# Kernel tuning notes

Measured on AMD Instinct MI355X. Metric: run time of the kernel, lower is better.

Reference implementation:

```python
import jax, jax.numpy as jnp
import numpy as np

EPS = 1e-8

def setup_inputs() -> dict:
    key = jax.random.key(0)
    kq, kk, kv = jax.random.split(key, 3)
    S, B, D = 2048, 8, 64
    return {
        "query": jax.random.normal(kq, (S, B, D), dtype=jnp.float32),
        "key": jax.random.normal(kk, (S, B, D), dtype=jnp.float32),
        "value": jax.random.normal(kv, (S, B, D), dtype=jnp.float32),
    }

def reference(query, key, value):
    # SWAP-test fidelity: expval(Z) = |<q_hat|k_hat>|^2, overlap = 0.5*(1+Z).
    # Zero-padding to 2**n_qubits does not change the inner product.
    q_hat = query / (jnp.linalg.norm(query, axis=-1, keepdims=True) + EPS)
    k_hat = key / (jnp.linalg.norm(key, axis=-1, keepdims=True) + EPS)
    # cosine similarity per batch: [B, S_q, S_k]
    cos = jnp.einsum('ibd,jbd->bij', q_hat, k_hat)
    overlap = 0.5 * (1.0 + cos * cos)
    attn_probs = jax.nn.softmax(overlap, axis=-1)          # [B, S, S]
    context = jnp.einsum('bij,jbd->ibd', attn_probs, value)  # [S, B, D]
    attn_weights = jnp.transpose(attn_probs, (1, 0, 2))      # [S, B, S]
    return context, attn_weights
```

## Files before the change

kernel.cpp:

```cpp
#include <hip/hip_runtime.h>

#define S_LEN 2048
#define BATCH 8
#define DIM   64
#define QT    16
#define KT    64
#define NT    32
#define NQT   128
#define PP    68
#define PBP   72
#define EPSV  1e-8f

#define WS_K_OFF (1u << 20)
#define WS_V_OFF (1u << 21)
#define WS_NEED_BYTES (6u * 1024u * 1024u)

typedef __attribute__((ext_vector_type(8))) short short8;
typedef __attribute__((ext_vector_type(4))) short short4v;
typedef __attribute__((ext_vector_type(4))) float f32x4;

__device__ __forceinline__ short bf16b(float x) {
    unsigned int u = __builtin_bit_cast(unsigned int, x);
    u = (u + 0x7fffu + ((u >> 16) & 1u)) >> 16;
    return (short)u;
}

__global__ __launch_bounds__(256)
void prep(const float* __restrict__ Qg, const float* __restrict__ Kg,
          const float* __restrict__ Vg, short* __restrict__ ws)
{
    const int blk = blockIdx.x;
    const int tid = threadIdx.x;
    if (blk < 512) {
        const bool isK = blk >= 256;
        const float* src = isK ? Kg : Qg;
        short* dst = ws + (isK ? WS_K_OFF : 0u);
        const int rg = (blk & 255) * 64 + (tid >> 2);
        const int rq = tid & 3;
        const int s = rg >> 3, b = rg & 7;
        const float4* rp = reinterpret_cast<const float4*>(src) + (size_t)rg * 16;
        float4 v[4];
        float ss = 0.f;
        #pragma unroll
        for (int c = 0; c < 4; ++c) {
            v[c] = rp[rq * 4 + c];
            ss += v[c].x*v[c].x + v[c].y*v[c].y + v[c].z*v[c].z + v[c].w*v[c].w;
        }
        ss += __shfl_xor(ss, 1);
        ss += __shfl_xor(ss, 2);
        const float sc = 1.f / (sqrtf(ss) + EPSV);
        const float* pf = reinterpret_cast<const float*>(v);
        #pragma unroll
        for (int h = 0; h < 2; ++h) {
            const int c8 = rq * 2 + h;
            const int kk = c8 >> 2, lg = c8 & 3;
            const int chunk = (b * NQT + (s >> 4)) * 128 + kk * 64 + lg * 16 + (s & 15);
            short8 o;
            #pragma unroll
            for (int j = 0; j < 8; ++j) o[j] = bf16b(pf[h * 8 + j] * sc);
            *reinterpret_cast<short8*>(dst + (size_t)chunk * 8) = o;
        }
    } else {
        const int cid = (blk - 512) * 256 + tid;
        const int l  = cid & 63;
        const int kk = (cid >> 6) & 1;
        const int gd = (cid >> 7) & 3;
        const int t  = (cid >> 9) & 31;
        const int b  = cid >> 14;
        const int d  = gd * 16 + (l & 15);
        const int k0 = t * 64 + kk * 32 + (l >> 4) * 8;
        short8 o;
        #pragma unroll
        for (int j = 0; j < 8; ++j)
            o[j] = bf16b(Vg[((size_t)(k0 + j) * BATCH + b) * DIM + d]);
        *reinterpret_cast<short8*>(ws + WS_V_OFF + (size_t)cid * 8) = o;
    }
}

__global__ __launch_bounds__(256, 4)
void qattn2(const short* __restrict__ Qp, const short* __restrict__ Kp,
            const short* __restrict__ Vp, float* __restrict__ out)
{
    __shared__ float Pf[QT * PP];
    __shared__ short Pb[QT * PBP];
    __shared__ float rsum[QT];

    const int tid = threadIdx.x;
    const int l   = tid & 63;
    const int w   = tid >> 6;
    const int lg  = l >> 4;
    const int lr  = l & 15;

    const int b     = blockIdx.x & 7;
    const int qt    = blockIdx.x >> 3;
    const int qbase = qt * QT;

    const short8* Qc = reinterpret_cast<const short8*>(Qp) + (size_t)(b * NQT + qt) * 128;
    const short8 aq0 = Qc[l];
    const short8 aq1 = Qc[64 + l];

    if (tid < QT) rsum[tid] = 0.f;
    __syncthreads();

    const short8* Kb = reinterpret_cast<const short8*>(Kp) + (size_t)b * NQT * 128;
    const short8* Vb = reinterpret_cast<const short8*>(Vp) + (size_t)b * NT * 4 * 128;

    float sums[4] = {0.f, 0.f, 0.f, 0.f};
    for (int t = 0; t < NT; ++t) {
        const short8* kc = Kb + (size_t)(4 * t + w) * 128 + l;
        const short8 k0 = kc[0];
        const short8 k1 = kc[64];
        f32x4 acc = {0.f, 0.f, 0.f, 0.f};
        acc = __builtin_amdgcn_mfma_f32_16x16x32_bf16(aq0, k0, acc, 0, 0, 0);
        acc = __builtin_amdgcn_mfma_f32_16x16x32_bf16(aq1, k1, acc, 0, 0, 0);
        #pragma unroll
        for (int r = 0; r < 4; ++r) {
            float c = acc[r];
            sums[r] += __expf(0.5f + 0.5f * c * c);
        }
    }
    #pragma unroll
    for (int r = 0; r < 4; ++r) {
        float v = sums[r];
        v += __shfl_xor(v, 1);
        v += __shfl_xor(v, 2);
        v += __shfl_xor(v, 4);
        v += __shfl_xor(v, 8);
        sums[r] = v;
    }
    if (lr == 0) {
        #pragma unroll
        for (int r = 0; r < 4; ++r)
            atomicAdd(&rsum[lg * 4 + r], sums[r]);
    }
    __syncthreads();
    float inv_[4];
    #pragma unroll
    for (int r = 0; r < 4; ++r) inv_[r] = 1.f / rsum[lg * 4 + r];

    float* attn = out + (size_t)S_LEN * BATCH * DIM;
    f32x4 cacc = {0.f, 0.f, 0.f, 0.f};

    short8 k0, k1;
    {
        const short8* kc = Kb + (size_t)w * 128 + l;
        k0 = kc[0]; k1 = kc[64];
    }

    for (int t = 0; t < NT; ++t) {
        const short8* vc = Vb + (size_t)(t * 4 + w) * 128 + l;
        const short8 v0 = vc[0];
        const short8 v1 = vc[64];
        const int tn = (t + 1 < NT) ? t + 1 : t;
        const short8* kc = Kb + (size_t)(4 * tn + w) * 128 + l;
        const short8 kn0 = kc[0];
        const short8 kn1 = kc[64];

        f32x4 acc = {0.f, 0.f, 0.f, 0.f};
        acc = __builtin_amdgcn_mfma_f32_16x16x32_bf16(aq0, k0, acc, 0, 0, 0);
        acc = __builtin_amdgcn_mfma_f32_16x16x32_bf16(aq1, k1, acc, 0, 0, 0);
        #pragma unroll
        for (int r = 0; r < 4; ++r) {
            float c = acc[r];
            float p = __expf(0.5f + 0.5f * c * c) * inv_[r];
            Pf[(lg * 4 + r) * PP + w * 16 + lr] = p;
            Pb[(lg * 4 + r) * PBP + w * 16 + lr] = bf16b(p);
        }
        asm volatile("s_waitcnt lgkmcnt(0)" ::: "memory");
        __builtin_amdgcn_sched_barrier(0);
        __builtin_amdgcn_s_barrier();
        __builtin_amdgcn_sched_barrier(0);

        const short8 ap0 = *reinterpret_cast<const short8*>(&Pb[lr * PBP + lg * 8]);
        const short8 ap1 = *reinterpret_cast<const short8*>(&Pb[lr * PBP + 32 + lg * 8]);
        cacc = __builtin_amdgcn_mfma_f32_16x16x32_bf16(ap0, v0, cacc, 0, 0, 0);
        cacc = __builtin_amdgcn_mfma_f32_16x16x32_bf16(ap1, v1, cacc, 0, 0, 0);

        {
            const int q  = tid >> 4;
            const int c4 = (tid & 15) * 4;
            f32x4 pv = *reinterpret_cast<const f32x4*>(&Pf[q * PP + c4]);
            __builtin_nontemporal_store(pv, reinterpret_cast<f32x4*>(
                attn + (size_t)(qbase + q) * (BATCH * S_LEN) + b * S_LEN + t * KT + c4));
        }
        asm volatile("s_waitcnt lgkmcnt(0)" ::: "memory");
        __builtin_amdgcn_sched_barrier(0);
        __builtin_amdgcn_s_barrier();
        __builtin_amdgcn_sched_barrier(0);

        k0 = kn0; k1 = kn1;
    }

    #pragma unroll
    for (int r = 0; r < 4; ++r) {
        out[(size_t)(qbase + lg * 4 + r) * (BATCH * DIM) + b * DIM + w * 16 + lr] = cacc[r];
    }
}

#define FQT 32
#define FQP 72
#define FPP 68

__global__ __launch_bounds__(256, 4)
void qattn_fb(const float* __restrict__ Qg, const float* __restrict__ Kg,
              const float* __restrict__ Vg, float* __restrict__ out)
{
    __shared__ short Qsh[FQT * FQP];
    __shared__ short Ksh[KT * FQP];
    __shared__ short VTs[DIM * FQP];
    __shared__ short Pb [FQT * FQP];
    __shared__ float Pf [FQT * FPP];
    __shared__ float rsum[FQT];

    const int tid = threadIdx.x;
    const int l   = tid & 63;
    const int w   = tid >> 6;
    const int lg  = l >> 4;
    const int lr  = l & 15;
    const int ms  = (w & 1) * 16;
    const int np  = (w >> 1) * 2;

    const int b     = blockIdx.x & 7;
    const int qtile = blockIdx.x >> 3;
    const int qbase = qtile * FQT;

    const int rr = tid >> 2;
    const int rq = tid & 3;

    if (tid < FQT * 4) {
        const float4* qp = reinterpret_cast<const float4*>(
            Qg + (size_t)(qbase + rr) * (BATCH * DIM) + b * DIM);
        float4 v[4];
        float ss = 0.f;
        #pragma unroll
        for (int c = 0; c < 4; ++c) {
            v[c] = qp[rq + 4 * c];
            ss += v[c].x*v[c].x + v[c].y*v[c].y + v[c].z*v[c].z + v[c].w*v[c].w;
        }
        ss += __shfl_xor(ss, 1);
        ss += __shfl_xor(ss, 2);
        const float sc = 1.f / (sqrtf(ss) + EPSV);
        #pragma unroll
        for (int c = 0; c < 4; ++c) {
            short4v s4 = { bf16b(v[c].x * sc), bf16b(v[c].y * sc),
                           bf16b(v[c].z * sc), bf16b(v[c].w * sc) };
            *reinterpret_cast<short4v*>(&Qsh[rr * FQP + rq * 4 + 16 * c]) = s4;
        }
    }
    if (tid < FQT) rsum[tid] = 0.f;
    __syncthreads();

    short8 aq[2];
    #pragma unroll
    for (int kk = 0; kk < 2; ++kk)
        aq[kk] = *reinterpret_cast<const short8*>(&Qsh[(ms + lr) * FQP + kk * 32 + lg * 8]);

    float sums[4] = {0.f, 0.f, 0.f, 0.f};
    for (int t = 0; t < NT; ++t) {
        __syncthreads();
        {
            const float4* kp = reinterpret_cast<const float4*>(
                Kg + (size_t)(t * KT + rr) * (BATCH * DIM) + b * DIM);
            float4 v[4];
            float ss = 0.f;
            #pragma unroll
            for (int c = 0; c < 4; ++c) {
                v[c] = kp[rq + 4 * c];
                ss += v[c].x*v[c].x + v[c].y*v[c].y + v[c].z*v[c].z + v[c].w*v[c].w;
            }
            ss += __shfl_xor(ss, 1);
            ss += __shfl_xor(ss, 2);
            const float sc = 1.f / (sqrtf(ss) + EPSV);
            #pragma unroll
            for (int c = 0; c < 4; ++c) {
                short4v s4 = { bf16b(v[c].x * sc), bf16b(v[c].y * sc),
                               bf16b(v[c].z * sc), bf16b(v[c].w * sc) };
                *reinterpret_cast<short4v*>(&Ksh[rr * FQP + rq * 4 + 16 * c]) = s4;
            }
        }
        __syncthreads();
        #pragma unroll
        for (int g = 0; g < 2; ++g) {
            f32x4 acc = {0.f, 0.f, 0.f, 0.f};
            #pragma unroll
            for (int kk = 0; kk < 2; ++kk) {
                short8 bk = *reinterpret_cast<const short8*>(
                    &Ksh[((np + g) * 16 + lr) * FQP + kk * 32 + lg * 8]);
                acc = __builtin_amdgcn_mfma_f32_16x16x32_bf16(aq[kk], bk, acc, 0, 0, 0);
            }
            #pragma unroll
            for (int r = 0; r < 4; ++r) {
                float c = acc[r];
                sums[r] += __expf(0.5f + 0.5f * c * c);
            }
        }
    }
    #pragma unroll
    for (int r = 0; r < 4; ++r) {
        float v = sums[r];
        v += __shfl_xor(v, 1);
        v += __shfl_xor(v, 2);
        v += __shfl_xor(v, 4);
        v += __shfl_xor(v, 8);
        sums[r] = v;
    }
    if (lr == 0) {
        #pragma unroll
        for (int r = 0; r < 4; ++r)
            atomicAdd(&rsum[ms + lg * 4 + r], sums[r]);
    }
    __syncthreads();
    float inv4[4];
    #pragma unroll
    for (int r = 0; r < 4; ++r)
        inv4[r] = 1.f / rsum[ms + lg * 4 + r];

    float* attn = out + (size_t)S_LEN * BATCH * DIM;
    f32x4 cacc[2];
    cacc[0] = (f32x4){0.f, 0.f, 0.f, 0.f};
    cacc[1] = (f32x4){0.f, 0.f, 0.f, 0.f};

    for (int t = 0; t < NT; ++t) {
        __syncthreads();
        {
            const float4* kp = reinterpret_cast<const float4*>(
                Kg + (size_t)(t * KT + rr) * (BATCH * DIM) + b * DIM);
            float4 v[4];
            float ss = 0.f;
            #pragma unroll
            for (int c = 0; c < 4; ++c) {
                v[c] = kp[rq + 4 * c];
                ss += v[c].x*v[c].x + v[c].y*v[c].y + v[c].z*v[c].z + v[c].w*v[c].w;
            }
            ss += __shfl_xor(ss, 1);
            ss += __shfl_xor(ss, 2);
            const float sc = 1.f / (sqrtf(ss) + EPSV);
            #pragma unroll
            for (int c = 0; c < 4; ++c) {
                short4v s4 = { bf16b(v[c].x * sc), bf16b(v[c].y * sc),
                               bf16b(v[c].z * sc), bf16b(v[c].w * sc) };
                *reinterpret_cast<short4v*>(&Ksh[rr * FQP + rq * 4 + 16 * c]) = s4;
            }
        }
        {
            const float4* vp = reinterpret_cast<const float4*>(
                Vg + (size_t)(t * KT + rr) * (BATCH * DIM) + b * DIM);
            #pragma unroll
            for (int c = 0; c < 4; ++c) {
                float4 v = vp[rq + 4 * c];
                int d0 = rq * 4 + 16 * c;
                VTs[(d0 + 0) * FQP + rr] = bf16b(v.x);
                VTs[(d0 + 1) * FQP + rr] = bf16b(v.y);
                VTs[(d0 + 2) * FQP + rr] = bf16b(v.z);
                VTs[(d0 + 3) * FQP + rr] = bf16b(v.w);
            }
        }
        __syncthreads();
        #pragma unroll
        for (int g = 0; g < 2; ++g) {
            f32x4 acc = {0.f, 0.f, 0.f, 0.f};
            #pragma unroll
            for (int kk = 0; kk < 2; ++kk) {
                short8 bk = *reinterpret_cast<const short8*>(
                    &Ksh[((np + g) * 16 + lr) * FQP + kk * 32 + lg * 8]);
                acc = __builtin_amdgcn_mfma_f32_16x16x32_bf16(aq[kk], bk, acc, 0, 0, 0);
            }
            #pragma unroll
            for (int r = 0; r < 4; ++r) {
                float c = acc[r];
                float p = __expf(0.5f + 0.5f * c * c) * inv4[r];
                int q_r = ms + lg * 4 + r;
                int k_c = (np + g) * 16 + lr;
                Pf[q_r * FPP + k_c] = p;
                Pb[q_r * FQP + k_c] = bf16b(p);
            }
        }
        __syncthreads();
        #pragma unroll
        for (int g = 0; g < 2; ++g) {
            #pragma unroll
            for (int kk = 0; kk < 2; ++kk) {
                short8 ap = *reinterpret_cast<const short8*>(
                    &Pb[(ms + lr) * FQP + kk * 32 + lg * 8]);
                short8 bv = *reinterpret_cast<const short8*>(
                    &VTs[((np + g) * 16 + lr) * FQP + kk * 32 + lg * 8]);
                cacc[g] = __builtin_amdgcn_mfma_f32_16x16x32_bf16(ap, bv, cacc[g], 0, 0, 0);
            }
        }
        #pragma unroll
        for (int s = 0; s < 2; ++s) {
            int q  = s * 16 + (tid >> 4);
            int c4 = (tid & 15) * 4;
            f32x4 pv = *reinterpret_cast<const f32x4*>(&Pf[q * FPP + c4]);
            __builtin_nontemporal_store(pv, reinterpret_cast<f32x4*>(
                attn + (size_t)(qbase + q) * (BATCH * S_LEN) + b * S_LEN + t * KT + c4));
        }
    }

    #pragma unroll
    for (int g = 0; g < 2; ++g) {
        #pragma unroll
        for (int r = 0; r < 4; ++r) {
            __builtin_nontemporal_store(cacc[g][r],
                out + (size_t)(qbase + ms + lg * 4 + r) * (BATCH * DIM)
                    + b * DIM + (np + g) * 16 + lr);
        }
    }
}

extern "C" void kernel_launch(void* const* d_in, const int* in_sizes, int n_in,
                              void* d_out, int out_size, void* d_ws, size_t ws_size,
                              hipStream_t stream)
{
    const float* q = (const float*)d_in[0];
    const float* k = (const float*)d_in[1];
    const float* v = (const float*)d_in[2];
    float* o  = (float*)d_out;

    if (ws_size >= WS_NEED_BYTES && d_ws != nullptr) {
        short* ws = (short*)d_ws;
        prep<<<1024, 256, 0, stream>>>(q, k, v, ws);
        qattn2<<<1024, 256, 0, stream>>>(ws, ws + WS_K_OFF, ws + WS_V_OFF, o);
    } else {
        qattn_fb<<<BATCH * (S_LEN / FQT), 256, 0, stream>>>(q, k, v, o);
    }
}
```

Baseline: 171.3 us.

## Enlarge attention tile to 32 queries x 128 keys with 8-wave blocks

Result: no change. 169.6 us (-1.0%).

```diff
diff --git a/kernel.cpp b/kernel.cpp
--- a/kernel.cpp
+++ b/kernel.cpp
@@ -3,12 +3,12 @@
 #define S_LEN 2048
 #define BATCH 8
 #define DIM   64
-#define QT    16
-#define KT    64
-#define NT    32
+#define QT    32
+#define KTILE 128
+#define NT2   16
 #define NQT   128
-#define PP    68
-#define PBP   72
+#define PP    132
+#define PBP   136
 #define EPSV  1e-8f
 
 #define WS_K_OFF (1u << 20)
@@ -24,6 +24,13 @@
     u = (u + 0x7fffu + ((u >> 16) & 1u)) >> 16;
     return (short)u;
 }
+
+#define LDS_BARRIER() do { \
+    asm volatile("s_waitcnt lgkmcnt(0)" ::: "memory"); \
+    __builtin_amdgcn_sched_barrier(0); \
+    __builtin_amdgcn_s_barrier(); \
+    __builtin_amdgcn_sched_barrier(0); \
+} while (0)
 
 __global__ __launch_bounds__(256)
 void prep(const float* __restrict__ Qg, const float* __restrict__ Kg,
@@ -77,8 +84,8 @@
     }
 }
 
-__global__ __launch_bounds__(256, 4)
-void qattn2(const short* __restrict__ Qp, const short* __restrict__ Kp,
+__global__ __launch_bounds__(512, 4)
+void qattn3(const short* __restrict__ Qp, const short* __restrict__ Kp,
             const short* __restrict__ Vp, float* __restrict__ out)
 {
     __shared__ float Pf[QT * PP];
@@ -90,33 +97,237 @@
     const int w   = tid >> 6;
     const int lg  = l >> 4;
     const int lr  = l & 15;
+    const int kg  = w;
+    const int ms  = (w >> 2) * 16;
+    const int dg  = w & 3;
 
     const int b     = blockIdx.x & 7;
     const int qt    = blockIdx.x >> 3;
     const int qbase = qt * QT;
 
-    const short8* Qc = reinterpret_cast<const short8*>(Qp) + (size_t)(b * NQT + qt) * 128;
-    const short8 aq0 = Qc[l];
-    const short8 aq1 = Qc[64 + l];
+    const short8* Qp8 = reinterpret_cast<const short8*>(Qp);
+    short8 aq[2][2];
+    #pragma unroll
+    for (int m = 0; m < 2; ++m) {
+        const size_t base = (size_t)(b * NQT + qt * 2 + m) * 128;
+        aq[m][0] = Qp8[base + l];
+        aq[m][1] = Qp8[base + 64 + l];
+    }
 
     if (tid < QT) rsum[tid] = 0.f;
     __syncthreads();
 
-    const short8* Kb = reinterpret_cast<const short8*>(Kp) + (size_t)b * NQT * 128;
-    const short8* Vb = reinterpret_cast<const short8*>(Vp) + (size_t)b * NT * 4 * 128;
+    const short8* Kb8 = reinterpret_cast<const short8*>(Kp) + (size_t)b * NQT * 128;
+    const short8* Vb8 = reinterpret_cast<const short8*>(Vp) + (size_t)b * 32 * 4 * 128;
+
+    float sums[2][4] = {{0.f,0.f,0.f,0.f},{0.f,0.f,0.f,0.f}};
+    short8 k0 = Kb8[(size_t)kg * 128 + l];
+    short8 k1 = Kb8[(size_t)kg * 128 + 64 + l];
+    for (int t = 0; t < NT2; ++t) {
+        const int tn = (t + 1 < NT2) ? t + 1 : t;
+        const short8* kc = &Kb8[(size_t)(8 * tn + kg) * 128 + l];
+        const short8 kn0 = kc[0];
+        const short8 kn1 = kc[64];
+        #pragma unroll
+        for (int m = 0; m < 2; ++m) {
+            f32x4 acc = {0.f, 0.f, 0.f, 0.f};
+            acc = __builtin_amdgcn_mfma_f32_16x16x32_bf16(aq[m][0], k0, acc, 0, 0, 0);
+            acc = __builtin_amdgcn_mfma_f32_16x16x32_bf16(aq[m][1], k1, acc, 0, 0, 0);
+            #pragma unroll
+            for (int r = 0; r < 4; ++r) {
+                float c = acc[r];
+                sums[m][r] += __expf(0.5f + 0.5f * c * c);
+            }
+        }
+        k0 = kn0; k1 = kn1;
+    }
+    #pragma unroll
+    for (int m = 0; m < 2; ++m)
+    #pragma unroll
+    for (int r = 0; r < 4; ++r) {
+        float v = sums[m][r];
+        v += __shfl_xor(v, 1);
+        v += __shfl_xor(v, 2);
+        v += __shfl_xor(v, 4);
+        v += __shfl_xor(v, 8);
+        sums[m][r] = v;
+    }
+    if (lr == 0) {
+        #pragma unroll
+        for (int m = 0; m < 2; ++m)
+        #pragma unroll
+        for (int r = 0; r < 4; ++r)
+            atomicAdd(&rsum[m * 16 + lg * 4 + r], sums[m][r]);
+    }
+    __syncthreads();
+    float inv_[2][4];
+    #pragma unroll
+    for (int m = 0; m < 2; ++m)
+    #pragma unroll
+    for (int r = 0; r < 4; ++r)
+        inv_[m][r] = 1.f / rsum[m * 16 + lg * 4 + r];
+
+    float* attn = out + (size_t)S_LEN * BATCH * DIM;
+    f32x4 cacc = {0.f, 0.f, 0.f, 0.f};
+
+    k0 = Kb8[(size_t)kg * 128 + l];
+    k1 = Kb8[(size_t)kg * 128 + 64 + l];
+
+    for (int t = 0; t < NT2; ++t) {
+        short8 bv[4];
+        #pragma unroll
+        for (int kk2 = 0; kk2 < 4; ++kk2) {
+            const int tv = t * 2 + (kk2 >> 1);
+            bv[kk2] = Vb8[(size_t)(tv * 4 + dg) * 128 + (kk2 & 1) * 64 + l];
+        }
+        const int tn = (t + 1 < NT2) ? t + 1 : t;
+        const short8* kc = &Kb8[(size_t)(8 * tn + kg) * 128 + l];
+        const short8 kn0 = kc[0];
+        const short8 kn1 = kc[64];
+
+        #pragma unroll
+        for (int m = 0; m < 2; ++m) {
+            f32x4 acc = {0.f, 0.f, 0.f, 0.f};
+            acc = __builtin_amdgcn_mfma_f32_16x16x32_bf16(aq[m][0], k0, acc, 0, 0, 0);
+            acc = __builtin_amdgcn_mfma_f32_16x16x32_bf16(aq[m][1], k1, acc, 0, 0, 0);
+            #pragma unroll
+            for (int r = 0; r < 4; ++r) {
+                float c = acc[r];
+                float p = __expf(0.5f + 0.5f * c * c) * inv_[m][r];
+                const int q_r = m * 16 + lg * 4 + r;
+                const int k_c = kg * 16 + lr;
+                Pf[q_r * PP + k_c] = p;
+                Pb[q_r * PBP + k_c] = bf16b(p);
+            }
+        }
+        LDS_BARRIER();
+
+        {
+            const int q = tid >> 4;
+            const int c = (tid & 15) * 4;
+            f32x4 pv0 = *reinterpret_cast<const f32x4*>(&Pf[q * PP + c]);
+            f32x4 pv1 = *reinterpret_cast<const f32x4*>(&Pf[q * PP + 64 + c]);
+            float* dst = attn + (size_t)(qbase + q) * (BATCH * S_LEN) + b * S_LEN + t * KTILE;
+            __builtin_nontemporal_store(pv0, reinterpret_cast<f32x4*>(dst + c));
+            __builtin_nontemporal_store(pv1, reinterpret_cast<f32x4*>(dst + 64 + c));
+        }
+
+        #pragma unroll
+        for (int kk2 = 0; kk2 < 4; ++kk2) {
+            const short8 ap = *reinterpret_cast<const short8*>(
+                &Pb[(ms + lr) * PBP + kk2 * 32 + lg * 8]);
+            cacc = __builtin_amdgcn_mfma_f32_16x16x32_bf16(ap, bv[kk2], cacc, 0, 0, 0);
+        }
+        LDS_BARRIER();
+
+        k0 = kn0; k1 = kn1;
+    }
+
+    #pragma unroll
+    for (int r = 0; r < 4; ++r) {
+        out[(size_t)(qbase + ms + lg * 4 + r) * (BATCH * DIM) + b * DIM + dg * 16 + lr]
+            = cacc[r];
+    }
+}
+
+#define FQT 32
+#define FQP 72
+#define FPP 68
+#define FKT 64
+#define FNT 32
+
+__global__ __launch_bounds__(256, 4)
+void qattn_fb(const float* __restrict__ Qg, const float* __restrict__ Kg,
+              const float* __restrict__ Vg, float* __restrict__ out)
+{
+    __shared__ short Qsh[FQT * FQP];
+    __shared__ short Ksh[FKT * FQP];
+    __shared__ short VTs[DIM * FQP];
+    __shared__ short Pb [FQT * FQP];
+    __shared__ float Pf [FQT * FPP];
+    __shared__ float rsum[FQT];
+
+    const int tid = threadIdx.x;
+    const int l   = tid & 63;
+    const int w   = tid >> 6;
+    const int lg  = l >> 4;
+    const int lr  = l & 15;
+    const int ms  = (w & 1) * 16;
+    const int np  = (w >> 1) * 2;
+
+    const int b     = blockIdx.x & 7;
+    const int qtile = blockIdx.x >> 3;
+    const int qbase = qtile * FQT;
+
+    const int rr = tid >> 2;
+    const int rq = tid & 3;
+
+    if (tid < FQT * 4) {
+        const float4* qp = reinterpret_cast<const float4*>(
+            Qg + (size_t)(qbase + rr) * (BATCH * DIM) + b * DIM);
+        float4 v[4];
+        float ss = 0.f;
+        #pragma unroll
+        for (int c = 0; c < 4; ++c) {
+            v[c] = qp[rq + 4 * c];
+            ss += v[c].x*v[c].x + v[c].y*v[c].y + v[c].z*v[c].z + v[c].w*v[c].w;
+        }
+        ss += __shfl_xor(ss, 1);
+        ss += __shfl_xor(ss, 2);
+        const float sc = 1.f / (sqrtf(ss) + EPSV);
+        #pragma unroll
+        for (int c = 0; c < 4; ++c) {
+            short4v s4 = { bf16b(v[c].x * sc), bf16b(v[c].y * sc),
+                           bf16b(v[c].z * sc), bf16b(v[c].w * sc) };
+            *reinterpret_cast<short4v*>(&Qsh[rr * FQP + rq * 4 + 16 * c]) = s4;
+        }
+    }
+    if (tid < FQT) rsum[tid] = 0.f;
+    __syncthreads();
+
+    short8 aq[2];
+    #pragma unroll
+    for (int kk = 0; kk < 2; ++kk)
+        aq[kk] = *reinterpret_cast<const short8*>(&Qsh[(ms + lr) * FQP + kk * 32 + lg * 8]);
 
     float sums[4] = {0.f, 0.f, 0.f, 0.f};
-    for (int t = 0; t < NT; ++t) {
-        const short8* kc = Kb + (size_t)(4 * t + w) * 128 + l;
-        const short8 k0 = kc[0];
-        const short8 k1 = kc[64];
-        f32x4 acc = {0.f, 0.f, 0.f, 0.f};
-        acc = __builtin_amdgcn_mfma_f32_16x16x32_bf16(aq0, k0, acc, 0, 0, 0);
-        acc = __builtin_amdgcn_mfma_f32_16x16x32_bf16(aq1, k1, acc, 0, 0, 0);
-        #pragma unroll
-        for (int r = 0; r < 4; ++r) {
-            float c = acc[r];
-            sums[r] += __expf(0.5f + 0.5f * c * c);
+    for (int t = 0; t < FNT; ++t) {
+        __syncthreads();
+        {
+            const float4* kp = reinterpret_cast<const float4*>(
+                Kg + (size_t)(t * FKT + rr) * (BATCH * DIM) + b * DIM);
+            float4 v[4];
+            float ss = 0.f;
+            #pragma unroll
+            for (int c = 0; c < 4; ++c) {
+                v[c] = kp[rq + 4 * c];
+                ss += v[c].x*v[c].x + v[c].y*v[c].y + v[c].z*v[c].z + v[c].w*v[c].w;
+            }
+            ss += __shfl_xor(ss, 1);
+            ss += __shfl_xor(ss, 2);
+            const float sc = 1.f / (sqrtf(ss) + EPSV);
+            #pragma unroll
+            for (int c = 0; c < 4; ++c) {
+                short4v s4 = { bf16b(v[c].x * sc), bf16b(v[c].y * sc),
+                               bf16b(v[c].z * sc), bf16b(v[c].w * sc) };
+                *reinterpret_cast<short4v*>(&Ksh[rr * FQP + rq * 4 + 16 * c]) = s4;
+            }
+        }
+        __syncthreads();
+        #pragma unroll
+        for (int g = 0; g < 2; ++g) {
+            f32x4 acc = {0.f, 0.f, 0.f, 0.f};
+            #pragma unroll
+            for (int kk = 0; kk < 2; ++kk) {
+                short8 bk = *reinterpret_cast<const short8*>(
+                    &Ksh[((np + g) * 16 + lr) * FQP + kk * 32 + lg * 8]);
+                acc = __builtin_amdgcn_mfma_f32_16x16x32_bf16(aq[kk], bk, acc, 0, 0, 0);
+            }
+            #pragma unroll
+            for (int r = 0; r < 4; ++r) {
+                float c = acc[r];
+                sums[r] += __expf(0.5f + 0.5f * c * c);
+            }
         }
     }
     #pragma unroll
@@ -131,136 +342,24 @@
     if (lr == 0) {
         #pragma unroll
         for (int r = 0; r < 4; ++r)
-            atomicAdd(&rsum[lg * 4 + r], sums[r]);
+            atomicAdd(&rsum[ms + lg * 4 + r], sums[r]);
     }
     __syncthreads();
-    float inv_[4];
-    #pragma unroll
-    for (int r = 0; r < 4; ++r) inv_[r] = 1.f / rsum[lg * 4 + r];
+    float inv4[4];
+    #pragma unroll
+    for (int r = 0; r < 4; ++r)
+        inv4[r] = 1.f / rsum[ms + lg * 4 + r];
 
     float* attn = out + (size_t)S_LEN * BATCH * DIM;
-    f32x4 cacc = {0.f, 0.f, 0.f, 0.f};
-
-    short8 k0, k1;
-    {
-        const short8* kc = Kb + (size_t)w * 128 + l;
-        k0 = kc[0]; k1 = kc[64];
-    }
-
-    for (int t = 0; t < NT; ++t) {
-        const short8* vc = Vb + (size_t)(t * 4 + w) * 128 + l;
-        const short8 v0 = vc[0];
-        const short8 v1 = vc[64];
-        const int tn = (t + 1 < NT) ? t + 1 : t;
-        const short8* kc = Kb + (size_t)(4 * tn + w) * 128 + l;
-        const short8 kn0 = kc[0];
-        const short8 kn1 = kc[64];
-
-        f32x4 acc = {0.f, 0.f, 0.f, 0.f};
-        acc = __builtin_amdgcn_mfma_f32_16x16x32_bf16(aq0, k0, acc, 0, 0, 0);
-        acc = __builtin_amdgcn_mfma_f32_16x16x32_bf16(aq1, k1, acc, 0, 0, 0);
-        #pragma unroll
-        for (int r = 0; r < 4; ++r) {
-            float c = acc[r];
-            float p = __expf(0.5f + 0.5f * c * c) * inv_[r];
-            Pf[(lg * 4 + r) * PP + w * 16 + lr] = p;
-            Pb[(lg * 4 + r) * PBP + w * 16 + lr] = bf16b(p);
-        }
-        asm volatile("s_waitcnt lgkmcnt(0)" ::: "memory");
-        __builtin_amdgcn_sched_barrier(0);
-        __builtin_amdgcn_s_barrier();
-        __builtin_amdgcn_sched_barrier(0);
-
-        const short8 ap0 = *reinterpret_cast<const short8*>(&Pb[lr * PBP + lg * 8]);
-        const short8 ap1 = *reinterpret_cast<const short8*>(&Pb[lr * PBP + 32 + lg * 8]);
-        cacc = __builtin_amdgcn_mfma_f32_16x16x32_bf16(ap0, v0, cacc, 0, 0, 0);
-        cacc = __builtin_amdgcn_mfma_f32_16x16x32_bf16(ap1, v1, cacc, 0, 0, 0);
-
-        {
-            const int q  = tid >> 4;
-            const int c4 = (tid & 15) * 4;
-            f32x4 pv = *reinterpret_cast<const f32x4*>(&Pf[q * PP + c4]);
-            __builtin_nontemporal_store(pv, reinterpret_cast<f32x4*>(
-                attn + (size_t)(qbase + q) * (BATCH * S_LEN) + b * S_LEN + t * KT + c4));
-        }
-        asm volatile("s_waitcnt lgkmcnt(0)" ::: "memory");
-        __builtin_amdgcn_sched_barrier(0);
-        __builtin_amdgcn_s_barrier();
-        __builtin_amdgcn_sched_barrier(0);
-
-        k0 = kn0; k1 = kn1;
-    }
-
-    #pragma unroll
-    for (int r = 0; r < 4; ++r) {
-        out[(size_t)(qbase + lg * 4 + r) * (BATCH * DIM) + b * DIM + w * 16 + lr] = cacc[r];
-    }
-}
-
-#define FQT 32
-#define FQP 72
-#define FPP 68
-
-__global__ __launch_bounds__(256, 4)
-void qattn_fb(const float* __restrict__ Qg, const float* __restrict__ Kg,
-              const float* __restrict__ Vg, float* __restrict__ out)
-{
-    __shared__ short Qsh[FQT * FQP];
-    __shared__ short Ksh[KT * FQP];
-    __shared__ short VTs[DIM * FQP];
-    __shared__ short Pb [FQT * FQP];
-    __shared__ float Pf [FQT * FPP];
-    __shared__ float rsum[FQT];
-
-    const int tid = threadIdx.x;
-    const int l   = tid & 63;
-    const int w   = tid >> 6;
-    const int lg  = l >> 4;
-    const int lr  = l & 15;
-    const int ms  = (w & 1) * 16;
-    const int np  = (w >> 1) * 2;
-
-    const int b     = blockIdx.x & 7;
-    const int qtile = blockIdx.x >> 3;
-    const int qbase = qtile * FQT;
-
-    const int rr = tid >> 2;
-    const int rq = tid & 3;
-
-    if (tid < FQT * 4) {
-        const float4* qp = reinterpret_cast<const float4*>(
-            Qg + (size_t)(qbase + rr) * (BATCH * DIM) + b * DIM);
-        float4 v[4];
-        float ss = 0.f;
-        #pragma unroll
-        for (int c = 0; c < 4; ++c) {
-            v[c] = qp[rq + 4 * c];
-            ss += v[c].x*v[c].x + v[c].y*v[c].y + v[c].z*v[c].z + v[c].w*v[c].w;
-        }
-        ss += __shfl_xor(ss, 1);
-        ss += __shfl_xor(ss, 2);
-        const float sc = 1.f / (sqrtf(ss) + EPSV);
-        #pragma unroll
-        for (int c = 0; c < 4; ++c) {
-            short4v s4 = { bf16b(v[c].x * sc), bf16b(v[c].y * sc),
-                           bf16b(v[c].z * sc), bf16b(v[c].w * sc) };
-            *reinterpret_cast<short4v*>(&Qsh[rr * FQP + rq * 4 + 16 * c]) = s4;
-        }
-    }
-    if (tid < FQT) rsum[tid] = 0.f;
-    __syncthreads();
-
-    short8 aq[2];
-    #pragma unroll
-    for (int kk = 0; kk < 2; ++kk)
-        aq[kk] = *reinterpret_cast<const short8*>(&Qsh[(ms + lr) * FQP + kk * 32 + lg * 8]);
-
-    float sums[4] = {0.f, 0.f, 0.f, 0.f};
-    for (int t = 0; t < NT; ++t) {
+    f32x4 cacc[2];
+    cacc[0] = (f32x4){0.f, 0.f, 0.f, 0.f};
+    cacc[1] = (f32x4){0.f, 0.f, 0.f, 0.f};
+
+    for (int t = 0; t < FNT; ++t) {
         __syncthreads();
         {
             const float4* kp = reinterpret_cast<const float4*>(
-                Kg + (size_t)(t * KT + rr) * (BATCH * DIM) + b * DIM);
+                Kg + (size_t)(t * FKT + rr) * (BATCH * DIM) + b * DIM);
             float4 v[4];
             float ss = 0.f;
             #pragma unroll
@@ -278,73 +377,9 @@
                 *reinterpret_cast<short4v*>(&Ksh[rr * FQP + rq * 4 + 16 * c]) = s4;
             }
         }
-        __syncthreads();
-        #pragma unroll
-        for (int g = 0; g < 2; ++g) {
-            f32x4 acc = {0.f, 0.f, 0.f, 0.f};
-            #pragma unroll
-            for (int kk = 0; kk < 2; ++kk) {
-                short8 bk = *reinterpret_cast<const short8*>(
-                    &Ksh[((np + g) * 16 + lr) * FQP + kk * 32 + lg * 8]);
-                acc = __builtin_amdgcn_mfma_f32_16x16x32_bf16(aq[kk], bk, acc, 0, 0, 0);
-            }
-            #pragma unroll
-            for (int r = 0; r < 4; ++r) {
-                float c = acc[r];
-                sums[r] += __expf(0.5f + 0.5f * c * c);
-            }
-        }
-    }
-    #pragma unroll
-    for (int r = 0; r < 4; ++r) {
-        float v = sums[r];
-        v += __shfl_xor(v, 1);
-        v += __shfl_xor(v, 2);
-        v += __shfl_xor(v, 4);
-        v += __shfl_xor(v, 8);
-        sums[r] = v;
-    }
-    if (lr == 0) {
-        #pragma unroll
-        for (int r = 0; r < 4; ++r)
-            atomicAdd(&rsum[ms + lg * 4 + r], sums[r]);
-    }
-    __syncthreads();
-    float inv4[4];
-    #pragma unroll
-    for (int r = 0; r < 4; ++r)
-        inv4[r] = 1.f / rsum[ms + lg * 4 + r];
-
-    float* attn = out + (size_t)S_LEN * BATCH * DIM;
-    f32x4 cacc[2];
-    cacc[0] = (f32x4){0.f, 0.f, 0.f, 0.f};
-    cacc[1] = (f32x4){0.f, 0.f, 0.f, 0.f};
-
-    for (int t = 0; t < NT; ++t) {
-        __syncthreads();
-        {
-            const float4* kp = reinterpret_cast<const float4*>(
-                Kg + (size_t)(t * KT + rr) * (BATCH * DIM) + b * DIM);
-            float4 v[4];
-            float ss = 0.f;
-            #pragma unroll
-            for (int c = 0; c < 4; ++c) {
-                v[c] = kp[rq + 4 * c];
-                ss += v[c].x*v[c].x + v[c].y*v[c].y + v[c].z*v[c].z + v[c].w*v[c].w;
-            }
-            ss += __shfl_xor(ss, 1);
-            ss += __shfl_xor(ss, 2);
-            const float sc = 1.f / (sqrtf(ss) + EPSV);
-            #pragma unroll
-            for (int c = 0; c < 4; ++c) {
-                short4v s4 = { bf16b(v[c].x * sc), bf16b(v[c].y * sc),
-                               bf16b(v[c].z * sc), bf16b(v[c].w * sc) };
-                *reinterpret_cast<short4v*>(&Ksh[rr * FQP + rq * 4 + 16 * c]) = s4;
-            }
-        }
         {
             const float4* vp = reinterpret_cast<const float4*>(
-                Vg + (size_t)(t * KT + rr) * (BATCH * DIM) + b * DIM);
+                Vg + (size_t)(t * FKT + rr) * (BATCH * DIM) + b * DIM);
             #pragma unroll
             for (int c = 0; c < 4; ++c) {
                 float4 v = vp[rq + 4 * c];
@@ -393,7 +428,7 @@
             int c4 = (tid & 15) * 4;
             f32x4 pv = *reinterpret_cast<const f32x4*>(&Pf[q * FPP + c4]);
             __builtin_nontemporal_store(pv, reinterpret_cast<f32x4*>(
-                attn + (size_t)(qbase + q) * (BATCH * S_LEN) + b * S_LEN + t * KT + c4));
+                attn + (size_t)(qbase + q) * (BATCH * S_LEN) + b * S_LEN + t * FKT + c4));
         }
     }
 
@@ -420,7 +455,7 @@
     if (ws_size >= WS_NEED_BYTES && d_ws != nullptr) {
         short* ws = (short*)d_ws;
         prep<<<1024, 256, 0, stream>>>(q, k, v, ws);
-        qattn2<<<1024, 256, 0, stream>>>(ws, ws + WS_K_OFF, ws + WS_V_OFF, o);
+        qattn3<<<BATCH * (S_LEN / QT), 512, 0, stream>>>(ws, ws + WS_K_OFF, ws + WS_V_OFF, o);
     } else {
         qattn_fb<<<BATCH * (S_LEN / FQT), 256, 0, stream>>>(q, k, v, o);
     }
```
